# Optimization experiments

Hardware: AMD Instinct MI355X
Metric: run time of the kernel (lower is better)

The kernel has to match this reference:

```python
import jax, jax.numpy as jnp
import numpy as np

N = 50000   # graph nodes (== num_edges of road network, Embedding vocab)
E = 800000  # message-passing edges
F = 64      # static_feat_dim
H = 256     # hidden_dim
ID = 32     # id_embed_dim
DYN = 16    # dyn_feat_dim
B = 256
T = 128
STEPS = 3   # gcn_iter


def setup_inputs():
    key = jax.random.key(0)
    it = iter(jax.random.split(key, 48))

    def nrm(shape, fan_in):
        return jax.random.normal(next(it), shape, jnp.float32) / np.sqrt(fan_in)

    edge_src = jax.random.randint(next(it), (E,), 0, N)
    edge_dst = jax.random.randint(next(it), (E,), 0, N)
    lengths = jax.random.randint(next(it), (B,), T // 2, T + 1)
    traj = jax.random.randint(next(it), (B, T), 1, N)
    mask = jnp.arange(T)[None, :] < lengths[:, None]
    traj = jnp.where(mask, traj, 0)  # padding idx 0 past length
    x0 = jax.random.normal(next(it), (N, F), jnp.float32)
    dyn_feat = jax.random.normal(next(it), (B, DYN), jnp.float32)
    Din = H + ID + DYN
    z = lambda *s: jnp.zeros(s, jnp.float32)
    inp = dict(
        x0=x0, dyn_feat=dyn_feat,
        Wproj=nrm((F, H), F), bproj=z(H),
        Wz=nrm((F + H, H), F + H), bz=z(H),
        Wr=nrm((F + H, H), F + H), br=z(H),
        Wn=nrm((F + H, H), F + H), bn=z(H),
        id_emb=nrm((N, ID), 1.0).at[0].set(0.0),  # padding_idx=0
        film_W1=nrm((DYN, H), DYN), film_b1=z(H),
        film_W2=nrm((H, 2 * H), H), film_b2=z(2 * H),
        gru_Wi_f=nrm((Din, 3 * H), Din), gru_Wh_f=nrm((H, 3 * H), H),
        gru_bi_f=z(3 * H), gru_bh_f=z(3 * H),
        gru_Wi_b=nrm((Din, 3 * H), Din), gru_Wh_b=nrm((H, 3 * H), H),
        gru_bi_b=z(3 * H), gru_bh_b=z(3 * H),
        ln_g=jnp.ones((2 * H,), jnp.float32), ln_b=z(2 * H),
        attn_W1=nrm((2 * H + DYN, H), 2 * H + DYN), attn_b1=z(H),
        attn_W2=nrm((H, 1), H), attn_b2=z(1),
        gate_W=nrm((4 * H + DYN, 2 * H), 4 * H + DYN), gate_b=z(2 * H),
        fc_W1=nrm((2 * H + DYN, H), 2 * H + DYN), fc_b1=z(H),
        fc_W2=nrm((H, 1), H), fc_b2=z(1),
        traj=traj, lengths=lengths, edge_src=edge_src, edge_dst=edge_dst)
    return inp


def _run_gru(x, mask, Wi, Wh, bi, bh):
    # x: [B,T,D]; mask: [B,T] bool. Returns (outs [B,T,H] zeroed past length,
    # h_last [B,H] = state at last valid step), matching packed torch GRU.
    xg = jnp.einsum('btd,dh->bth', x, Wi) + bi  # precompute input gates
    Hd = Wh.shape[0]

    def step(h, inp):
        gx, m = inp
        gh = h @ Wh + bh
        xr, xz, xn = jnp.split(gx, 3, axis=-1)
        hr, hz, hn = jnp.split(gh, 3, axis=-1)
        r = jax.nn.sigmoid(xr + hr)
        zt = jax.nn.sigmoid(xz + hz)
        n = jnp.tanh(xn + r * hn)
        h_new = (1 - zt) * n + zt * h
        m2 = m[:, None]
        h = jnp.where(m2, h_new, h)
        return h, h * m2

    h0 = jnp.zeros((x.shape[0], Hd), x.dtype)
    h_last, outs = jax.lax.scan(step, h0, (jnp.swapaxes(xg, 0, 1), mask.T))
    return jnp.swapaxes(outs, 0, 1), h_last


def _forward(x0, dyn_feat, Wproj, bproj, Wz, bz, Wr, br, Wn, bn, id_emb,
             film_W1, film_b1, film_W2, film_b2,
             gru_Wi_f, gru_Wh_f, gru_bi_f, gru_bh_f,
             gru_Wi_b, gru_Wh_b, gru_bi_b, gru_bh_b,
             ln_g, ln_b, attn_W1, attn_b1, attn_W2, attn_b2,
             gate_W, gate_b, fc_W1, fc_b1, fc_W2, fc_b2,
             traj, lengths, edge_src, edge_dst):
    # --- GGNN message passing: scatter-add aggregation + gated update ---
    h = jnp.tanh(x0 @ Wproj + bproj)  # [N,H]
    for _ in range(STEPS):
        h_agg = jax.ops.segment_sum(h[edge_src], edge_dst, num_segments=N)
        xc = jnp.concatenate([x0, h_agg], axis=1)
        zg = jax.nn.sigmoid(xc @ Wz + bz)
        rg = jax.nn.sigmoid(xc @ Wr + br)
        h_t = jnp.tanh(jnp.concatenate([x0, rg * h_agg], axis=1) @ Wn + bn)
        h = (1 - zg) * h_agg + zg * h_t
    # --- FiLM-modulated trajectory sequence ---
    x_seq = h[traj]  # [B,T,H]
    film = jnp.tanh((dyn_feat @ film_W1 + film_b1) @ film_W2 + film_b2)
    g, b = jnp.split(film, 2, axis=-1)
    x_seq = x_seq * (1 + g[:, None, :]) + b[:, None, :]
    dyn_exp = jnp.broadcast_to(dyn_feat[:, None, :], (B, T, DYN))
    rnn_in = jnp.concatenate([x_seq, id_emb[traj], dyn_exp], axis=-1)
    mask = jnp.arange(T)[None, :] < lengths[:, None]
    # --- BiGRU over packed (length-masked) sequences ---
    out_f, h_f = _run_gru(rnn_in, mask, gru_Wi_f, gru_Wh_f, gru_bi_f, gru_bh_f)
    rev = jnp.maximum(lengths[:, None] - 1 - jnp.arange(T)[None, :], 0)  # [B,T]
    x_rev = jnp.take_along_axis(rnn_in, rev[..., None], axis=1)
    out_rb, h_b = _run_gru(x_rev, mask, gru_Wi_b, gru_Wh_b, gru_bi_b, gru_bh_b)
    out_b = jnp.take_along_axis(out_rb, rev[..., None], axis=1) * mask[..., None]
    rnn_out = jnp.concatenate([out_f, out_b], axis=-1)  # [B,T,2H]
    h_last = jnp.concatenate([h_f, h_b], axis=1)        # [B,2H]
    mu = h_last.mean(-1, keepdims=True)
    var = ((h_last - mu) ** 2).mean(-1, keepdims=True)
    rnn_last = (h_last - mu) / jnp.sqrt(var + 1e-5) * ln_g + ln_b
    # --- attention pooling over valid steps ---
    score_in = jnp.concatenate([rnn_out, dyn_exp], axis=-1)
    scores = (jnp.tanh(score_in @ attn_W1 + attn_b1) @ attn_W2 + attn_b2)[..., 0]
    scores = jnp.where(traj != 0, scores, -1e9)
    alpha = jax.nn.softmax(scores, axis=1)[..., None]
    context = (rnn_out * alpha).sum(axis=1)
    # --- fusion gate + head ---
    gate_in = jnp.concatenate([context, rnn_last, dyn_feat], axis=1)
    zf = jax.nn.sigmoid(gate_in @ gate_W + gate_b)
    final = zf * context + (1 - zf) * rnn_last
    hfc = jax.nn.gelu(jnp.concatenate([final, dyn_feat], axis=1) @ fc_W1 + fc_b1,
                      approximate=False)
    return (hfc @ fc_W2 + fc_b2)[:, 0]


def reference(x0, dyn_feat, Wproj, bproj, Wz, bz, Wr, br, Wn, bn, id_emb,
              film_W1, film_b1, film_W2, film_b2,
              gru_Wi_f, gru_Wh_f, gru_bi_f, gru_bh_f,
              gru_Wi_b, gru_Wh_b, gru_bi_b, gru_bh_b,
              ln_g, ln_b, attn_W1, attn_b1, attn_W2, attn_b2,
              gate_W, gate_b, fc_W1, fc_b1, fc_W2, fc_b2,
              traj, lengths, edge_src, edge_dst):
    return _forward(x0, dyn_feat, Wproj, bproj, Wz, bz, Wr, br, Wn, bn, id_emb,
                    film_W1, film_b1, film_W2, film_b2,
                    gru_Wi_f, gru_Wh_f, gru_bi_f, gru_bh_f,
                    gru_Wi_b, gru_Wh_b, gru_bi_b, gru_bh_b,
                    ln_g, ln_b, attn_W1, attn_b1, attn_W2, attn_b2,
                    gate_W, gate_b, fc_W1, fc_b1, fc_W2, fc_b2,
                    traj, lengths, edge_src, edge_dst)
```

## Files before the change

kernel.cpp:

```cpp
#include <hip/hip_runtime.h>
#include <hip/hip_fp16.h>
#include <cmath>

#define NN   50000
#define EE   800000
#define FF   64
#define HH   256
#define IDD  32
#define DYNN 16
#define BB   256
#define TT   128
#define DIN  304
#define G3   768
#define NQ   (HH/4)
#define NQG  ((FF+HH)/4)
#define NQX  (DIN/4)

typedef _Float16 h2_t __attribute__((ext_vector_type(2)));
__device__ __forceinline__ float sigf(float x){ return 1.0f/(1.0f+expf(-x)); }
__device__ __forceinline__ float fdot2(__half2 a, __half2 b, float c) {
    return __builtin_amdgcn_fdot2(*reinterpret_cast<h2_t*>(&a),
                                  *reinterpret_cast<h2_t*>(&b), c, false);
}

#define NPB 16
__global__ __launch_bounds__(256) void k_proj(
    const float* __restrict__ x0, const float* __restrict__ Wproj,
    const float* __restrict__ bproj, float* __restrict__ h,
    __half* __restrict__ h16)
{
    __shared__ float xs[NPB][FF];
    int n0 = blockIdx.x * NPB;
    int j  = threadIdx.x;
    for (int i = j; i < NPB*FF; i += 256) {
        int m = i / FF, k = i % FF;
        int n = n0 + m;
        xs[m][k] = (n < NN) ? x0[n*FF + k] : 0.f;
    }
    __syncthreads();
    float acc[NPB];
#pragma unroll
    for (int m = 0; m < NPB; ++m) acc[m] = 0.f;
    for (int k = 0; k < FF; ++k) {
        float w = Wproj[k*HH + j];
#pragma unroll
        for (int m = 0; m < NPB; ++m) acc[m] += xs[m][k]*w;
    }
    float b = bproj[j];
#pragma unroll
    for (int m = 0; m < NPB; ++m) {
        int n = n0 + m;
        if (n < NN) {
            float v = tanhf(acc[m] + b);
            h[(size_t)n*HH + j] = v;
            h16[(size_t)n*HH + j] = __float2half(v);
        }
    }
}

__global__ __launch_bounds__(768) void k_wt2(
    const float* __restrict__ Wh, __half2* __restrict__ Wq)
{
    int q = blockIdx.x;
    int j = threadIdx.x;
    float w0 = Wh[(size_t)(4*q+0)*G3 + j];
    float w1 = Wh[(size_t)(4*q+1)*G3 + j];
    float w2 = Wh[(size_t)(4*q+2)*G3 + j];
    float w3 = Wh[(size_t)(4*q+3)*G3 + j];
    Wq[((size_t)q*G3 + j)*2 + 0] = __floats2half2_rn(w0, w1);
    Wq[((size_t)q*G3 + j)*2 + 1] = __floats2half2_rn(w2, w3);
}

__global__ __launch_bounds__(256) void k_wtg(
    const float* __restrict__ W, float2* __restrict__ Wq)
{
    int q = blockIdx.x;
    int j = threadIdx.x;
    __half2 a = __floats2half2_rn(W[(size_t)(4*q+0)*HH + j], W[(size_t)(4*q+1)*HH + j]);
    __half2 b = __floats2half2_rn(W[(size_t)(4*q+2)*HH + j], W[(size_t)(4*q+3)*HH + j]);
    float2 o;
    reinterpret_cast<__half2*>(&o)[0] = a;
    reinterpret_cast<__half2*>(&o)[1] = b;
    Wq[(size_t)q*HH + j] = o;
}

__global__ __launch_bounds__(768) void k_wti(
    const float* __restrict__ Wi, float2* __restrict__ Wq)
{
    int q = blockIdx.x;
    int j = threadIdx.x;
    __half2 a = __floats2half2_rn(Wi[(size_t)(4*q+0)*G3 + j], Wi[(size_t)(4*q+1)*G3 + j]);
    __half2 b = __floats2half2_rn(Wi[(size_t)(4*q+2)*G3 + j], Wi[(size_t)(4*q+3)*G3 + j]);
    float2 o;
    reinterpret_cast<__half2*>(&o)[0] = a;
    reinterpret_cast<__half2*>(&o)[1] = b;
    Wq[(size_t)q*G3 + j] = o;
}

__global__ __launch_bounds__(256) void k_hist(
    const int* __restrict__ dst, int* __restrict__ cnt)
{
    int e = blockIdx.x*256 + threadIdx.x;
    if (e < EE) atomicAdd(&cnt[dst[e]], 1);
}

__global__ __launch_bounds__(1024) void k_prefix(
    const int* __restrict__ cnt, int* __restrict__ offs)
{
    __shared__ int sm[1024];
    __shared__ int carry;
    int j = threadIdx.x;
    if (j == 0) carry = 0;
    __syncthreads();
    for (int base = 0; base < NN; base += 1024) {
        int v = (base + j < NN) ? cnt[base + j] : 0;
        sm[j] = v; __syncthreads();
        for (int s = 1; s < 1024; s <<= 1) {
            int t = (j >= s) ? sm[j - s] : 0;
            __syncthreads();
            sm[j] += t;
            __syncthreads();
        }
        int inc = sm[j];
        int c = carry;
        if (base + j < NN) offs[base + j] = c + inc - v;
        __syncthreads();
        if (j == 1023) carry = c + sm[1023];
        __syncthreads();
    }
    if (j == 0) offs[NN] = carry;
}

__global__ __launch_bounds__(256) void k_fill(
    const int* __restrict__ src, const int* __restrict__ dst,
    const int* __restrict__ offs, int* __restrict__ cur,
    int* __restrict__ srcb)
{
    int e = blockIdx.x*256 + threadIdx.x;
    if (e < EE) {
        int d = dst[e];
        int p = atomicAdd(&cur[d], 1);
        srcb[offs[d] + p] = src[e];
    }
}

#define APB 4
__global__ __launch_bounds__(256) void k_aggregate(
    const __half* __restrict__ h16, const int* __restrict__ offs,
    const int* __restrict__ srcb, float* __restrict__ hagg)
{
    int w    = threadIdx.x >> 6;
    int lane = threadIdx.x & 63;
    int n = blockIdx.x * APB + w;
    if (n >= NN) return;
    int e0 = offs[n], e1 = offs[n+1];
    float4 acc = {0.f, 0.f, 0.f, 0.f};
    int e = e0;
    for (; e + 4 <= e1; e += 4) {
        int s0 = srcb[e], s1 = srcb[e+1], s2 = srcb[e+2], s3 = srcb[e+3];
        float2 r0 = *reinterpret_cast<const float2*>(&h16[(size_t)s0*HH + lane*4]);
        float2 r1 = *reinterpret_cast<const float2*>(&h16[(size_t)s1*HH + lane*4]);
        float2 r2 = *reinterpret_cast<const float2*>(&h16[(size_t)s2*HH + lane*4]);
        float2 r3 = *reinterpret_cast<const float2*>(&h16[(size_t)s3*HH + lane*4]);
#pragma unroll
        for (int u = 0; u < 4; ++u) {
            float2* rp = (u==0)?&r0:(u==1)?&r1:(u==2)?&r2:&r3;
            float2 a = __half22float2(reinterpret_cast<__half2*>(rp)[0]);
            float2 b = __half22float2(reinterpret_cast<__half2*>(rp)[1]);
            acc.x += a.x; acc.y += a.y; acc.z += b.x; acc.w += b.y;
        }
    }
    for (; e < e1; ++e) {
        int s = srcb[e];
        float2 r = *reinterpret_cast<const float2*>(&h16[(size_t)s*HH + lane*4]);
        float2 a = __half22float2(reinterpret_cast<__half2*>(&r)[0]);
        float2 b = __half22float2(reinterpret_cast<__half2*>(&r)[1]);
        acc.x += a.x; acc.y += a.y; acc.z += b.x; acc.w += b.y;
    }
    *reinterpret_cast<float4*>(&hagg[(size_t)n*HH + lane*4]) = acc;
}

__global__ __launch_bounds__(256) void k_gnn_update(
    const float* __restrict__ x0, const float* __restrict__ hagg,
    const float2* __restrict__ wqz, const float2* __restrict__ wqr,
    const float2* __restrict__ wqn,
    const float* __restrict__ bz, const float* __restrict__ br,
    const float* __restrict__ bn, float* __restrict__ h,
    __half* __restrict__ h16)
{
    __shared__ __align__(16) __half inh[NPB][FF+HH];
    __shared__ __align__(16) __half rhh[NPB][HH];
    __shared__ float hsf[NPB][HH];
    int n0 = blockIdx.x * NPB;
    int j  = threadIdx.x;
    for (int i = j; i < NPB*FF; i += 256) {
        int m = i >> 6, k = i & 63;
        int n = n0 + m;
        inh[m][k] = __float2half((n < NN) ? x0[n*FF + k] : 0.f);
    }
#pragma unroll
    for (int m = 0; m < NPB; ++m) {
        int n = n0 + m;
        float hv = (n < NN) ? hagg[(size_t)n*HH + j] : 0.f;
        hsf[m][j] = hv;
        inh[m][FF + j] = __float2half(hv);
    }
    __syncthreads();

    float az[NPB], ar[NPB];
#pragma unroll
    for (int m = 0; m < NPB; ++m) { az[m] = 0.f; ar[m] = 0.f; }
    for (int q = 0; q < NQG; ++q) {
        float2 wzr = wqz[(size_t)q*HH + j];
        float2 wrr = wqr[(size_t)q*HH + j];
        __half2 wz01 = reinterpret_cast<__half2*>(&wzr)[0];
        __half2 wz23 = reinterpret_cast<__half2*>(&wzr)[1];
        __half2 wr01 = reinterpret_cast<__half2*>(&wrr)[0];
        __half2 wr23 = reinterpret_cast<__half2*>(&wrr)[1];
#pragma unroll
        for (int m = 0; m < NPB; ++m) {
            float2 hraw = *reinterpret_cast<const float2*>(&inh[m][4*q]);
            __half2 h01 = reinterpret_cast<__half2*>(&hraw)[0];
            __half2 h23 = reinterpret_cast<__half2*>(&hraw)[1];
            az[m] = fdot2(h01, wz01, az[m]); az[m] = fdot2(h23, wz23, az[m]);
            ar[m] = fdot2(h01, wr01, ar[m]); ar[m] = fdot2(h23, wr23, ar[m]);
        }
    }
    float bzj = bz[j], brj = br[j];
    float zg[NPB];
#pragma unroll
    for (int m = 0; m < NPB; ++m) {
        zg[m] = sigf(az[m] + bzj);
        float rg = sigf(ar[m] + brj);
        rhh[m][j] = __float2half(rg * hsf[m][j]);
    }
    __syncthreads();
    float an[NPB];
#pragma unroll
    for (int m = 0; m < NPB; ++m) an[m] = 0.f;
    for (int q = 0; q < FF/4; ++q) {
        float2 wnr = wqn[(size_t)q*HH + j];
        __half2 wn01 = reinterpret_cast<__half2*>(&wnr)[0];
        __half2 wn23 = reinterpret_cast<__half2*>(&wnr)[1];
#pragma unroll
        for (int m = 0; m < NPB; ++m) {
            float2 hraw = *reinterpret_cast<const float2*>(&inh[m][4*q]);
            __half2 h01 = reinterpret_cast<__half2*>(&hraw)[0];
            __half2 h23 = reinterpret_cast<__half2*>(&hraw)[1];
            an[m] = fdot2(h01, wn01, an[m]); an[m] = fdot2(h23, wn23, an[m]);
        }
    }
    for (int q = FF/4; q < NQG; ++q) {
        float2 wnr = wqn[(size_t)q*HH + j];
        __half2 wn01 = reinterpret_cast<__half2*>(&wnr)[0];
        __half2 wn23 = reinterpret_cast<__half2*>(&wnr)[1];
#pragma unroll
        for (int m = 0; m < NPB; ++m) {
            float2 hraw = *reinterpret_cast<const float2*>(&rhh[m][4*q - FF]);
            __half2 h01 = reinterpret_cast<__half2*>(&hraw)[0];
            __half2 h23 = reinterpret_cast<__half2*>(&hraw)[1];
            an[m] = fdot2(h01, wn01, an[m]); an[m] = fdot2(h23, wn23, an[m]);
        }
    }
    float bnj = bn[j];
#pragma unroll
    for (int m = 0; m < NPB; ++m) {
        int n = n0 + m;
        if (n < NN) {
            float ht = tanhf(an[m] + bnj);
            float hv = (1.f - zg[m])*hsf[m][j] + zg[m]*ht;
            h[(size_t)n*HH + j] = hv;
            h16[(size_t)n*HH + j] = __float2half(hv);
        }
    }
}

__global__ __launch_bounds__(256) void k_film(
    const float* __restrict__ dyn, const float* __restrict__ W1,
    const float* __restrict__ b1, const float* __restrict__ W2,
    const float* __restrict__ b2, float* __restrict__ film)
{
    __shared__ float t1[HH];
    __shared__ float ds[DYNN];
    int b = blockIdx.x, j = threadIdx.x;
    if (j < DYNN) ds[j] = dyn[b*DYNN + j];
    __syncthreads();
    float acc = b1[j];
    for (int k = 0; k < DYNN; ++k) acc += ds[k]*W1[k*HH + j];
    t1[j] = acc;
    __syncthreads();
    float a0 = b2[j], a1 = b2[HH + j];
    for (int k = 0; k < HH; ++k) {
        float t = t1[k];
        a0 += t * W2[k*2*HH + j];
        a1 += t * W2[k*2*HH + HH + j];
    }
    film[b*2*HH + j]      = tanhf(a0);
    film[b*2*HH + HH + j] = tanhf(a1);
}

#define RPB 16
#define XGBLK ((BB*TT)/RPB)
__global__ __launch_bounds__(256) void k_xg2(
    const float* __restrict__ hfin, const float* __restrict__ id_emb,
    const float* __restrict__ dyn,  const float* __restrict__ film,
    const int* __restrict__ traj,   const int* __restrict__ lengths,
    const float2* __restrict__ Wqi_f, const float* __restrict__ bi_f,
    const float2* __restrict__ Wqi_b, const float* __restrict__ bi_b,
    __half* __restrict__ xg_f, __half* __restrict__ xg_b)
{
    __shared__ __align__(16) __half in[RPB][DIN];
    int dir = blockIdx.x / XGBLK;
    int r0  = (blockIdx.x - dir*XGBLK) * RPB;
    const float2* Wq = dir ? Wqi_b : Wqi_f;
    const float* bi = dir ? bi_b : bi_f;
    __half* xg = dir ? xg_b : xg_f;
    int j  = threadIdx.x;
#pragma unroll
    for (int m = 0; m < RPB; ++m) {
        int r = r0 + m;
        int b = r >> 7, t = r & 127;
        int tt = t;
        if (dir) { int L = lengths[b]; tt = L - 1 - t; if (tt < 0) tt = 0; }
        int idx = traj[b*TT + tt];
        float g  = film[b*2*HH + j];
        float bf = film[b*2*HH + HH + j];
        in[m][j] = __float2half(hfin[(size_t)idx*HH + j]*(1.f + g) + bf);
        if (j < IDD)               in[m][HH + j] = __float2half(id_emb[(size_t)idx*IDD + j]);
        else if (j < IDD + DYNN)   in[m][HH + IDD + (j - IDD)] = __float2half(dyn[b*DYNN + (j - IDD)]);
    }
    __syncthreads();
    float a0[RPB], a1[RPB], a2[RPB];
#pragma unroll
    for (int m = 0; m < RPB; ++m) { a0[m] = 0.f; a1[m] = 0.f; a2[m] = 0.f; }
    for (int q = 0; q < NQX; ++q) {
        float2 w0r = Wq[(size_t)q*G3 + j];
        float2 w1r = Wq[(size_t)q*G3 + HH + j];
        float2 w2r = Wq[(size_t)q*G3 + 2*HH + j];
        __half2 w0a = reinterpret_cast<__half2*>(&w0r)[0];
        __half2 w0b = reinterpret_cast<__half2*>(&w0r)[1];
        __half2 w1a = reinterpret_cast<__half2*>(&w1r)[0];
        __half2 w1b = reinterpret_cast<__half2*>(&w1r)[1];
        __half2 w2a = reinterpret_cast<__half2*>(&w2r)[0];
        __half2 w2b = reinterpret_cast<__half2*>(&w2r)[1];
#pragma unroll
        for (int m = 0; m < RPB; ++m) {
            float2 hraw = *reinterpret_cast<const float2*>(&in[m][4*q]);
            __half2 h01 = reinterpret_cast<__half2*>(&hraw)[0];
            __half2 h23 = reinterpret_cast<__half2*>(&hraw)[1];
            a0[m] = fdot2(h01, w0a, a0[m]); a0[m] = fdot2(h23, w0b, a0[m]);
            a1[m] = fdot2(h01, w1a, a1[m]); a1[m] = fdot2(h23, w1b, a1[m]);
            a2[m] = fdot2(h01, w2a, a2[m]); a2[m] = fdot2(h23, w2b, a2[m]);
        }
    }
    float bi0 = bi[j], bi1 = bi[HH + j], bi2 = bi[2*HH + j];
#pragma unroll
    for (int m = 0; m < RPB; ++m) {
        __half* o = &xg[(size_t)(r0 + m)*G3];
        o[j]        = __float2half(a0[m] + bi0);
        o[HH + j]   = __float2half(a1[m] + bi1);
        o[2*HH + j] = __float2half(a2[m] + bi2);
    }
}

#define NBS 2
#define SCBLK (BB/NBS)
__global__ __launch_bounds__(768) void k_scan2(
    const __half* __restrict__ xg_f, const __half* __restrict__ xg_b,
    const __half2* __restrict__ Wq_f, const float* __restrict__ bh_f,
    const __half2* __restrict__ Wq_b, const float* __restrict__ bh_b,
    const int* __restrict__ lengths,
    float* __restrict__ out_f, float* __restrict__ out_b,
    float* __restrict__ h_last)
{
    __shared__ float hsh[NBS][HH];
    __shared__ __align__(16) __half hshh[NBS][HH];
    __shared__ float gh[NBS][G3];
    int dir  = blockIdx.x / SCBLK;
    int bblk = blockIdx.x - dir*SCBLK;
    const __half* xg = dir ? xg_b : xg_f;
    const __half2* Wq = dir ? Wq_b : Wq_f;
    const float* bh = dir ? bh_b : bh_f;
    float* out = dir ? out_b : out_f;
    int b0 = bblk * NBS;
    int j  = threadIdx.x;
    int m  = j >> 8;
    int jj = j & 255;
    if (j < NBS*HH) { hsh[j >> 8][j & 255] = 0.f; hshh[j >> 8][j & 255] = __float2half(0.f); }
    int L0 = lengths[b0], L1 = lengths[b0 + 1];
    float bhj = bh[j];
    const float2* wqp = reinterpret_cast<const float2*>(Wq) + j;
    float2 wreg[NQ];
#pragma unroll
    for (int q = 0; q < NQ; ++q) wreg[q] = wqp[(size_t)q*G3];
    __syncthreads();
    for (int t = 0; t < TT; ++t) {
        float xrv = 0.f, xzv = 0.f, xnv = 0.f;
        if (j < NBS*HH) {
            const __half* xr = &xg[((size_t)(b0 + m)*TT + t)*G3];
            xrv = __half2float(xr[jj]);
            xzv = __half2float(xr[HH + jj]);
            xnv = __half2float(xr[2*HH + jj]);
        }
        float a0 = bhj, a1 = bhj;
#pragma unroll
        for (int p = 0; p < NQ/2; ++p) {
            float4 h0raw = *reinterpret_cast<const float4*>(&hshh[0][8*p]);
            float4 h1raw = *reinterpret_cast<const float4*>(&hshh[1][8*p]);
            const __half2* h0 = reinterpret_cast<const __half2*>(&h0raw);
            const __half2* h1 = reinterpret_cast<const __half2*>(&h1raw);
            float2 w0 = wreg[2*p], w1 = wreg[2*p+1];
            const __half2* wA = reinterpret_cast<const __half2*>(&w0);
            const __half2* wB = reinterpret_cast<const __half2*>(&w1);
            a0 = fdot2(h0[0], wA[0], a0); a0 = fdot2(h0[1], wA[1], a0);
            a0 = fdot2(h0[2], wB[0], a0); a0 = fdot2(h0[3], wB[1], a0);
            a1 = fdot2(h1[0], wA[0], a1); a1 = fdot2(h1[1], wA[1], a1);
            a1 = fdot2(h1[2], wB[0], a1); a1 = fdot2(h1[3], wB[1], a1);
        }
        gh[0][j] = a0; gh[1][j] = a1;
        __syncthreads();
        if (j < NBS*HH) {
            int b = b0 + m;
            int L = m ? L1 : L0;
            float gr = sigf(xrv + gh[m][jj]);
            float gz = sigf(xzv + gh[m][HH + jj]);
            float gn = tanhf(xnv + gr*gh[m][2*HH + jj]);
            float hold = hsh[m][jj];
            float hnew = (1.f - gz)*gn + gz*hold;
            if (t < L) {
                hsh[m][jj] = hnew;
                hshh[m][jj] = __float2half(hnew);
                if (!dir) out[((size_t)b*TT + t)*HH + jj] = hnew;
                else      out[((size_t)b*TT + (L-1-t))*HH + jj] = hnew;
            } else if (!dir) {
                out[((size_t)b*TT + t)*HH + jj] = 0.f;
            }
        }
        __syncthreads();
    }
    if (j < NBS*HH) {
        int b = b0 + m;
        int L = m ? L1 : L0;
        h_last[b*2*HH + (dir ? HH : 0) + jj] = hsh[m][jj];
        if (dir) {
            for (int t = L; t < TT; ++t) out[((size_t)b*TT + t)*HH + jj] = 0.f;
        }
    }
}

#define SPB 16
#define SCD 528
__global__ __launch_bounds__(256) void k_scores(
    const float* __restrict__ out_f, const float* __restrict__ out_b,
    const float* __restrict__ dyn,   const int* __restrict__ traj,
    const float* __restrict__ W1,    const float* __restrict__ b1,
    const float* __restrict__ W2,    const float* __restrict__ b2,
    float* __restrict__ scores)
{
    __shared__ float in[SPB][SCD];
    __shared__ float part[4][SPB];
    int r0 = blockIdx.x * SPB;
    int j  = threadIdx.x;
    int lane = j & 63, wid = j >> 6;
#pragma unroll
    for (int m = 0; m < SPB; ++m) {
        int r = r0 + m;
        int b = r >> 7;
        in[m][j]      = out_f[(size_t)r*HH + j];
        in[m][HH + j] = out_b[(size_t)r*HH + j];
        if (j < DYNN) in[m][2*HH + j] = dyn[b*DYNN + j];
    }
    __syncthreads();
    float acc[SPB];
#pragma unroll
    for (int m = 0; m < SPB; ++m) acc[m] = 0.f;
    for (int k = 0; k < SCD; ++k) {
        float w = W1[k*HH + j];
#pragma unroll
        for (int m = 0; m < SPB; ++m) acc[m] += in[m][k]*w;
    }
    float b1j = b1[j], w2j = W2[j];
#pragma unroll
    for (int m = 0; m < SPB; ++m) {
        float s = tanhf(acc[m] + b1j) * w2j;
#pragma unroll
        for (int off = 32; off > 0; off >>= 1) s += __shfl_xor(s, off, 64);
        if (lane == 0) part[wid][m] = s;
    }
    __syncthreads();
    if (j < SPB) {
        int r = r0 + j;
        int b = r >> 7, t = r & 127;
        float s = part[0][j] + part[1][j] + part[2][j] + part[3][j];
        scores[r] = (traj[b*TT + t] != 0) ? (s + b2[0]) : -1e9f;
    }
}

__global__ __launch_bounds__(256) void k_context(
    const float* __restrict__ scores, const float* __restrict__ out_f,
    const float* __restrict__ out_b,  float* __restrict__ context)
{
    __shared__ float al[TT];
    __shared__ float red[256];
    int b = blockIdx.x, j = threadIdx.x;
    float s = (j < TT) ? scores[b*TT + j] : -INFINITY;
    red[j] = s; __syncthreads();
    for (int t = 128; t > 0; t >>= 1) { if (j < t) red[j] = fmaxf(red[j], red[j+t]); __syncthreads(); }
    float mx = red[0]; __syncthreads();
    float e = (j < TT) ? expf(s - mx) : 0.f;
    red[j] = e; __syncthreads();
    for (int t = 128; t > 0; t >>= 1) { if (j < t) red[j] += red[j+t]; __syncthreads(); }
    float tot = red[0];
    if (j < TT) al[j] = e / tot;
    __syncthreads();
    float c0 = 0.f, c1 = 0.f;
    for (int t = 0; t < TT; ++t) {
        float a = al[t];
        c0 += a * out_f[((size_t)b*TT + t)*HH + j];
        c1 += a * out_b[((size_t)b*TT + t)*HH + j];
    }
    context[b*2*HH + j]      = c0;
    context[b*2*HH + HH + j] = c1;
}

__global__ __launch_bounds__(256) void k_head(
    const float* __restrict__ h_last, const float* __restrict__ context,
    const float* __restrict__ dyn,    const float* __restrict__ ln_g,
    const float* __restrict__ ln_b,   const float* __restrict__ gate_W,
    const float* __restrict__ gate_b, const float* __restrict__ fc_W1,
    const float* __restrict__ fc_b1,  const float* __restrict__ fc_W2,
    const float* __restrict__ fc_b2,  float* __restrict__ outp)
{
    __shared__ float gi[1040];
    __shared__ float fin[SCD];
    __shared__ float red[256];
    int b = blockIdx.x, j = threadIdx.x;
    float h0 = h_last[b*2*HH + j], h1 = h_last[b*2*HH + HH + j];
    red[j] = h0 + h1; __syncthreads();
    for (int s = 128; s > 0; s >>= 1) { if (j < s) red[j] += red[j+s]; __syncthreads(); }
    float mu = red[0] / 512.f; __syncthreads();
    float d0 = h0 - mu, d1 = h1 - mu;
    red[j] = d0*d0 + d1*d1; __syncthreads();
    for (int s = 128; s > 0; s >>= 1) { if (j < s) red[j] += red[j+s]; __syncthreads(); }
    float inv = rsqrtf(red[0] / 512.f + 1e-5f); __syncthreads();
    gi[2*HH + j]      = d0*inv*ln_g[j]      + ln_b[j];
    gi[2*HH + HH + j] = d1*inv*ln_g[HH + j] + ln_b[HH + j];
    gi[j]      = context[b*2*HH + j];
    gi[HH + j] = context[b*2*HH + HH + j];
    if (j < DYNN) gi[1024 + j] = dyn[b*DYNN + j];
    __syncthreads();
    float a0 = gate_b[j], a1 = gate_b[HH + j];
    for (int k = 0; k < 1040; ++k) {
        float x = gi[k];
        a0 += x * gate_W[k*2*HH + j];
        a1 += x * gate_W[k*2*HH + HH + j];
    }
    float z0 = sigf(a0), z1 = sigf(a1);
    fin[j]      = z0*gi[j]      + (1.f - z0)*gi[2*HH + j];
    fin[HH + j] = z1*gi[HH + j] + (1.f - z1)*gi[2*HH + HH + j];
    if (j < DYNN) fin[2*HH + j] = gi[1024 + j];
    __syncthreads();
    float acc = fc_b1[j];
    for (int k = 0; k < SCD; ++k) acc += fin[k]*fc_W1[k*HH + j];
    float x = acc;
    float hfc = 0.5f * x * (1.f + erff(x * 0.70710678118654752f));
    red[j] = hfc * fc_W2[j]; __syncthreads();
    for (int s = 128; s > 0; s >>= 1) { if (j < s) red[j] += red[j+s]; __syncthreads(); }
    if (j == 0) outp[b] = red[0] + fc_b2[0];
}

extern "C" void kernel_launch(void* const* d_in, const int* in_sizes, int n_in,
                              void* d_out, int out_size, void* d_ws, size_t ws_size,
                              hipStream_t stream)
{
    const float* x0      = (const float*)d_in[0];
    const float* dyn     = (const float*)d_in[1];
    const float* Wproj   = (const float*)d_in[2];
    const float* bproj   = (const float*)d_in[3];
    const float* Wz      = (const float*)d_in[4];
    const float* bz      = (const float*)d_in[5];
    const float* Wr      = (const float*)d_in[6];
    const float* br      = (const float*)d_in[7];
    const float* Wn      = (const float*)d_in[8];
    const float* bn      = (const float*)d_in[9];
    const float* id_emb  = (const float*)d_in[10];
    const float* film_W1 = (const float*)d_in[11];
    const float* film_b1 = (const float*)d_in[12];
    const float* film_W2 = (const float*)d_in[13];
    const float* film_b2 = (const float*)d_in[14];
    const float* gWi_f   = (const float*)d_in[15];
    const float* gWh_f   = (const float*)d_in[16];
    const float* gbi_f   = (const float*)d_in[17];
    const float* gbh_f   = (const float*)d_in[18];
    const float* gWi_b   = (const float*)d_in[19];
    const float* gWh_b   = (const float*)d_in[20];
    const float* gbi_b   = (const float*)d_in[21];
    const float* gbh_b   = (const float*)d_in[22];
    const float* ln_g    = (const float*)d_in[23];
    const float* ln_b    = (const float*)d_in[24];
    const float* attn_W1 = (const float*)d_in[25];
    const float* attn_b1 = (const float*)d_in[26];
    const float* attn_W2 = (const float*)d_in[27];
    const float* attn_b2 = (const float*)d_in[28];
    const float* gate_W  = (const float*)d_in[29];
    const float* gate_b  = (const float*)d_in[30];
    const float* fc_W1   = (const float*)d_in[31];
    const float* fc_b1   = (const float*)d_in[32];
    const float* fc_W2   = (const float*)d_in[33];
    const float* fc_b2   = (const float*)d_in[34];
    const int*   traj    = (const int*)d_in[35];
    const int*   lengths = (const int*)d_in[36];
    const int*   e_src   = (const int*)d_in[37];
    const int*   e_dst   = (const int*)d_in[38];

    float* ws = (float*)d_ws;
    const size_t off_h      = 0;
    const size_t off_hagg   = (size_t)NN*HH;
    const size_t off_xgf    = off_hagg;
    const size_t off_xgb    = off_xgf + (size_t)BB*TT*G3/2;
    const size_t off_outf   = 0;
    const size_t off_outb   = off_xgb + (size_t)BB*TT*G3/2;
    const size_t off_film   = off_outb + (size_t)BB*TT*HH;
    const size_t off_hlast  = off_film + (size_t)BB*2*HH;
    const size_t off_scores = off_hlast + (size_t)BB*2*HH;
    const size_t off_ctx    = off_scores + (size_t)BB*TT;
    const size_t off_wqf    = off_ctx + (size_t)BB*2*HH;
    const size_t off_wqb    = off_wqf + (size_t)NQ*G3*2;
    const size_t off_wqz    = off_wqb + (size_t)NQ*G3*2;
    const size_t off_wqr    = off_wqz + (size_t)NQG*HH*2;
    const size_t off_wqn    = off_wqr + (size_t)NQG*HH*2;
    const size_t off_wif    = off_wqn + (size_t)NQG*HH*2;
    const size_t off_wib    = off_wif + (size_t)NQX*G3*2;
    const size_t off_h16    = 27000000;

    float*   h      = ws + off_h;
    float*   hagg   = ws + off_hagg;
    __half*  xg_f   = (__half*)(ws + off_xgf);
    __half*  xg_b   = (__half*)(ws + off_xgb);
    float*   out_f  = ws + off_outf;
    float*   out_b  = ws + off_outb;
    float*   film   = ws + off_film;
    float*   hlast  = ws + off_hlast;
    float*   scores = ws + off_scores;
    float*   ctx    = ws + off_ctx;
    __half2* wq_f   = (__half2*)(ws + off_wqf);
    __half2* wq_b   = (__half2*)(ws + off_wqb);
    float2*  wqz    = (float2*)(ws + off_wqz);
    float2*  wqr    = (float2*)(ws + off_wqr);
    float2*  wqn    = (float2*)(ws + off_wqn);
    float2*  wqi_f  = (float2*)(ws + off_wif);
    float2*  wqi_b  = (float2*)(ws + off_wib);
    __half*  h16    = (__half*)(ws + off_h16);

    int* cnt  = (int*)(ws + off_hagg + (size_t)NN*HH);
    int* cur  = cnt + NN;
    int* offs = cur + NN;
    int* srcb = offs + NN + 1;

    k_proj<<<(NN + NPB - 1)/NPB, 256, 0, stream>>>(x0, Wproj, bproj, h, h16);

    k_wt2<<<NQ, 768, 0, stream>>>(gWh_f, wq_f);
    k_wt2<<<NQ, 768, 0, stream>>>(gWh_b, wq_b);
    k_wtg<<<NQG, 256, 0, stream>>>(Wz, wqz);
    k_wtg<<<NQG, 256, 0, stream>>>(Wr, wqr);
    k_wtg<<<NQG, 256, 0, stream>>>(Wn, wqn);
    k_wti<<<NQX, 768, 0, stream>>>(gWi_f, wqi_f);
    k_wti<<<NQX, 768, 0, stream>>>(gWi_b, wqi_b);

    hipMemsetAsync(cnt, 0, 2*(size_t)NN*sizeof(int), stream);
    k_hist<<<(EE + 255)/256, 256, 0, stream>>>(e_dst, cnt);
    k_prefix<<<1, 1024, 0, stream>>>(cnt, offs);
    k_fill<<<(EE + 255)/256, 256, 0, stream>>>(e_src, e_dst, offs, cur, srcb);

    for (int step = 0; step < 3; ++step) {
        k_aggregate<<<(NN + APB - 1)/APB, 256, 0, stream>>>(h16, offs, srcb, hagg);
        k_gnn_update<<<(NN + NPB - 1)/NPB, 256, 0, stream>>>(
            x0, hagg, wqz, wqr, wqn, bz, br, bn, h, h16);
    }

    k_film<<<BB, 256, 0, stream>>>(dyn, film_W1, film_b1, film_W2, film_b2, film);

    k_xg2<<<2*XGBLK, 256, 0, stream>>>(h, id_emb, dyn, film, traj, lengths,
                                       wqi_f, gbi_f, wqi_b, gbi_b, xg_f, xg_b);

    k_scan2<<<2*SCBLK, 768, 0, stream>>>(xg_f, xg_b, wq_f, gbh_f, wq_b, gbh_b,
                                         lengths, out_f, out_b, hlast);

    k_scores<<<(BB*TT)/SPB, 256, 0, stream>>>(out_f, out_b, dyn, traj,
                                              attn_W1, attn_b1, attn_W2, attn_b2, scores);
    k_context<<<BB, 256, 0, stream>>>(scores, out_f, out_b, ctx);
    k_head<<<BB, 256, 0, stream>>>(hlast, ctx, dyn, ln_g, ln_b, gate_W, gate_b,
                                   fc_W1, fc_b1, fc_W2, fc_b2, (float*)d_out);
}
```

Baseline: 2.253 ms.

## Fuse neighbor aggregation into GNN update kernel with ping-pong half buffers

```diff
diff --git a/kernel.cpp b/kernel.cpp
--- a/kernel.cpp
+++ b/kernel.cpp
@@ -144,49 +144,14 @@
     }
 }
 
-#define APB 4
-__global__ __launch_bounds__(256) void k_aggregate(
-    const __half* __restrict__ h16, const int* __restrict__ offs,
-    const int* __restrict__ srcb, float* __restrict__ hagg)
-{
-    int w    = threadIdx.x >> 6;
-    int lane = threadIdx.x & 63;
-    int n = blockIdx.x * APB + w;
-    if (n >= NN) return;
-    int e0 = offs[n], e1 = offs[n+1];
-    float4 acc = {0.f, 0.f, 0.f, 0.f};
-    int e = e0;
-    for (; e + 4 <= e1; e += 4) {
-        int s0 = srcb[e], s1 = srcb[e+1], s2 = srcb[e+2], s3 = srcb[e+3];
-        float2 r0 = *reinterpret_cast<const float2*>(&h16[(size_t)s0*HH + lane*4]);
-        float2 r1 = *reinterpret_cast<const float2*>(&h16[(size_t)s1*HH + lane*4]);
-        float2 r2 = *reinterpret_cast<const float2*>(&h16[(size_t)s2*HH + lane*4]);
-        float2 r3 = *reinterpret_cast<const float2*>(&h16[(size_t)s3*HH + lane*4]);
-#pragma unroll
-        for (int u = 0; u < 4; ++u) {
-            float2* rp = (u==0)?&r0:(u==1)?&r1:(u==2)?&r2:&r3;
-            float2 a = __half22float2(reinterpret_cast<__half2*>(rp)[0]);
-            float2 b = __half22float2(reinterpret_cast<__half2*>(rp)[1]);
-            acc.x += a.x; acc.y += a.y; acc.z += b.x; acc.w += b.y;
-        }
-    }
-    for (; e < e1; ++e) {
-        int s = srcb[e];
-        float2 r = *reinterpret_cast<const float2*>(&h16[(size_t)s*HH + lane*4]);
-        float2 a = __half22float2(reinterpret_cast<__half2*>(&r)[0]);
-        float2 b = __half22float2(reinterpret_cast<__half2*>(&r)[1]);
-        acc.x += a.x; acc.y += a.y; acc.z += b.x; acc.w += b.y;
-    }
-    *reinterpret_cast<float4*>(&hagg[(size_t)n*HH + lane*4]) = acc;
-}
-
-__global__ __launch_bounds__(256) void k_gnn_update(
-    const float* __restrict__ x0, const float* __restrict__ hagg,
+__global__ __launch_bounds__(256) void k_gnn_fused(
+    const float* __restrict__ x0, const __half* __restrict__ h16in,
+    const int* __restrict__ offs, const int* __restrict__ srcb,
     const float2* __restrict__ wqz, const float2* __restrict__ wqr,
     const float2* __restrict__ wqn,
     const float* __restrict__ bz, const float* __restrict__ br,
     const float* __restrict__ bn, float* __restrict__ h,
-    __half* __restrict__ h16)
+    __half* __restrict__ h16out)
 {
     __shared__ __align__(16) __half inh[NPB][FF+HH];
     __shared__ __align__(16) __half rhh[NPB][HH];
@@ -198,12 +163,42 @@
         int n = n0 + m;
         inh[m][k] = __float2half((n < NN) ? x0[n*FF + k] : 0.f);
     }
-#pragma unroll
-    for (int m = 0; m < NPB; ++m) {
+    int wv = j >> 6, lane = j & 63;
+    for (int s = 0; s < 4; ++s) {
+        int m = wv*4 + s;
         int n = n0 + m;
-        float hv = (n < NN) ? hagg[(size_t)n*HH + j] : 0.f;
-        hsf[m][j] = hv;
-        inh[m][FF + j] = __float2half(hv);
+        float4 acc = {0.f, 0.f, 0.f, 0.f};
+        if (n < NN) {
+            int e0 = offs[n], e1 = offs[n+1];
+            int e = e0;
+            for (; e + 4 <= e1; e += 4) {
+                int s0 = srcb[e], s1 = srcb[e+1], s2 = srcb[e+2], s3 = srcb[e+3];
+                float2 r0 = *reinterpret_cast<const float2*>(&h16in[(size_t)s0*HH + lane*4]);
+                float2 r1 = *reinterpret_cast<const float2*>(&h16in[(size_t)s1*HH + lane*4]);
+                float2 r2 = *reinterpret_cast<const float2*>(&h16in[(size_t)s2*HH + lane*4]);
+                float2 r3 = *reinterpret_cast<const float2*>(&h16in[(size_t)s3*HH + lane*4]);
+#pragma unroll
+                for (int u = 0; u < 4; ++u) {
+                    float2* rp = (u==0)?&r0:(u==1)?&r1:(u==2)?&r2:&r3;
+                    float2 a = __half22float2(reinterpret_cast<__half2*>(rp)[0]);
+                    float2 b = __half22float2(reinterpret_cast<__half2*>(rp)[1]);
+                    acc.x += a.x; acc.y += a.y; acc.z += b.x; acc.w += b.y;
+                }
+            }
+            for (; e < e1; ++e) {
+                int sx = srcb[e];
+                float2 r = *reinterpret_cast<const float2*>(&h16in[(size_t)sx*HH + lane*4]);
+                float2 a = __half22float2(reinterpret_cast<__half2*>(&r)[0]);
+                float2 b = __half22float2(reinterpret_cast<__half2*>(&r)[1]);
+                acc.x += a.x; acc.y += a.y; acc.z += b.x; acc.w += b.y;
+            }
+        }
+        hsf[m][lane*4+0] = acc.x; hsf[m][lane*4+1] = acc.y;
+        hsf[m][lane*4+2] = acc.z; hsf[m][lane*4+3] = acc.w;
+        inh[m][FF+lane*4+0] = __float2half(acc.x);
+        inh[m][FF+lane*4+1] = __float2half(acc.y);
+        inh[m][FF+lane*4+2] = __float2half(acc.z);
+        inh[m][FF+lane*4+3] = __float2half(acc.w);
     }
     __syncthreads();
 
@@ -270,7 +265,7 @@
             float ht = tanhf(an[m] + bnj);
             float hv = (1.f - zg[m])*hsf[m][j] + zg[m]*ht;
             h[(size_t)n*HH + j] = hv;
-            h16[(size_t)n*HH + j] = __float2half(hv);
+            h16out[(size_t)n*HH + j] = __float2half(hv);
         }
     }
 }
@@ -365,7 +360,7 @@
 
 #define NBS 2
 #define SCBLK (BB/NBS)
-__global__ __launch_bounds__(768) void k_scan2(
+__global__ __launch_bounds__(768, 3) void k_scan2(
     const __half* __restrict__ xg_f, const __half* __restrict__ xg_b,
     const __half2* __restrict__ Wq_f, const float* __restrict__ bh_f,
     const __half2* __restrict__ Wq_b, const float* __restrict__ bh_b,
@@ -631,10 +626,10 @@
     const size_t off_wqn    = off_wqr + (size_t)NQG*HH*2;
     const size_t off_wif    = off_wqn + (size_t)NQG*HH*2;
     const size_t off_wib    = off_wif + (size_t)NQX*G3*2;
-    const size_t off_h16    = 27000000;
+    const size_t off_h16a   = 27000000;
+    const size_t off_h16b   = off_outb;
 
     float*   h      = ws + off_h;
-    float*   hagg   = ws + off_hagg;
     __half*  xg_f   = (__half*)(ws + off_xgf);
     __half*  xg_b   = (__half*)(ws + off_xgb);
     float*   out_f  = ws + off_outf;
@@ -650,14 +645,15 @@
     float2*  wqn    = (float2*)(ws + off_wqn);
     float2*  wqi_f  = (float2*)(ws + off_wif);
     float2*  wqi_b  = (float2*)(ws + off_wib);
-    __half*  h16    = (__half*)(ws + off_h16);
+    __half*  h16a   = (__half*)(ws + off_h16a);
+    __half*  h16b   = (__half*)(ws + off_h16b);
 
     int* cnt  = (int*)(ws + off_hagg + (size_t)NN*HH);
     int* cur  = cnt + NN;
     int* offs = cur + NN;
     int* srcb = offs + NN + 1;
 
-    k_proj<<<(NN + NPB - 1)/NPB, 256, 0, stream>>>(x0, Wproj, bproj, h, h16);
+    k_proj<<<(NN + NPB - 1)/NPB, 256, 0, stream>>>(x0, Wproj, bproj, h, h16a);
 
     k_wt2<<<NQ, 768, 0, stream>>>(gWh_f, wq_f);
     k_wt2<<<NQ, 768, 0, stream>>>(gWh_b, wq_b);
@@ -672,10 +668,11 @@
     k_prefix<<<1, 1024, 0, stream>>>(cnt, offs);
     k_fill<<<(EE + 255)/256, 256, 0, stream>>>(e_src, e_dst, offs, cur, srcb);
 
+    const __half* hin = h16a; __half* hout = h16b;
     for (int step = 0; step < 3; ++step) {
-        k_aggregate<<<(NN + APB - 1)/APB, 256, 0, stream>>>(h16, offs, srcb, hagg);
-        k_gnn_update<<<(NN + NPB - 1)/NPB, 256, 0, stream>>>(
-            x0, hagg, wqz, wqr, wqn, bz, br, bn, h, h16);
+        k_gnn_fused<<<(NN + NPB - 1)/NPB, 256, 0, stream>>>(
+            x0, hin, offs, srcb, wqz, wqr, wqn, bz, br, bn, h, hout);
+        const __half* tmp = hin; hin = hout; hout = (__half*)tmp;
     }
 
     k_film<<<BB, 256, 0, stream>>>(dyn, film_W1, film_b1, film_W2, film_b2, film);
```

New measurement: 2.272 ms. Within noise of the previous version (+0.8%).
